# Kernel optimization log

Hardware: AMD Instinct MI355X
Metric: run time of the kernel (lower is better)

Reference implementation:

```python
import jax, jax.numpy as jnp
import numpy as np

NUM_HEADS = 12
SIZE_PER_HEAD = 64


def setup_inputs() -> dict:
    key = jax.random.key(0)
    ks = jax.random.split(key, 4)
    B, S, D = 4, 2048, NUM_HEADS * SIZE_PER_HEAD
    std = 0.02
    return {
        "x": jax.random.normal(ks[0], (B, S, D), dtype=jnp.float32),
        "Wq": jax.random.normal(ks[1], (D, D), dtype=jnp.float32) * std,
        "bq": jnp.zeros((D,), dtype=jnp.float32),
        "Wk": jax.random.normal(ks[2], (D, D), dtype=jnp.float32) * std,
        "bk": jnp.zeros((D,), dtype=jnp.float32),
        "Wv": jax.random.normal(ks[3], (D, D), dtype=jnp.float32) * std,
        "bv": jnp.zeros((D,), dtype=jnp.float32),
        "mask": jnp.ones((B, S), dtype=jnp.int32),
    }


def reference(x, Wq, bq, Wk, bk, Wv, bv, mask):
    B, S, Dm = x.shape
    H, Dh = NUM_HEADS, SIZE_PER_HEAD
    # QKV projections (no activation, per defaults)
    q = (x @ Wq + bq).reshape(B, S, H, Dh)
    k = (x @ Wk + bk).reshape(B, S, H, Dh)
    v = (x @ Wv + bv).reshape(B, S, H, Dh)
    # scaled dot-product scores [B, H, F, T]
    scores = jnp.einsum("bfhd,bthd->bhft", q, k) / jnp.sqrt(
        jnp.asarray(Dh, dtype=x.dtype)
    )
    # additive mask: (1 - mask) * -10000, broadcast over heads and F
    adder = (1.0 - mask.astype(x.dtype))[:, None, None, :] * -10000.0
    probs = jax.nn.softmax(scores + adder, axis=-1)
    # dropout is identity at inference (training=None)
    ctx = jnp.einsum("bhft,bthd->bfhd", probs, v)
    return ctx.reshape(B, S, H * Dh)
```

## Files before the change

kernel.cpp:

```cpp
#include <hip/hip_runtime.h>
#include <cstdint>
#include <cstddef>

#define B_  4
#define S_  2048
#define H_  12
#define DH  64
#define DM  768

typedef unsigned short u16;
typedef __bf16 bf16x8 __attribute__((ext_vector_type(8)));
typedef float f32x4 __attribute__((ext_vector_type(4)));

__device__ __forceinline__ u16 f2bf(float f) {
  unsigned u = __float_as_uint(f);
  u += 0x7FFFu + ((u >> 16) & 1u);
  return (u16)(u >> 16);
}

__device__ __forceinline__ void gl16(const u16* g, u16* l) {
  __builtin_amdgcn_global_load_lds((const __attribute__((address_space(1))) void*)g,
                                   (__attribute__((address_space(3))) void*)l,
                                   16, 0, 0);
}

__global__ __launch_bounds__(256) void k_cvt_x(const float* __restrict__ x, u16* __restrict__ xb,
                                               const int* __restrict__ mask, int* __restrict__ mflags) {
  int i = blockIdx.x * 256 + threadIdx.x;
  const float4 v = ((const float4*)x)[i];
  ushort4 o;
  o.x = f2bf(v.x); o.y = f2bf(v.y); o.z = f2bf(v.z); o.w = f2bf(v.w);
  ((ushort4*)xb)[i] = o;
  if (blockIdx.x < 64) {
    __shared__ int f;
    if (threadIdx.x == 0) f = 0;
    __syncthreads();
    if (threadIdx.x < 128 && mask[blockIdx.x * 128 + threadIdx.x] != 1) f = 1;
    __syncthreads();
    if (threadIdx.x == 0) mflags[blockIdx.x] = f;
  }
}

__global__ __launch_bounds__(256) void k_wtrans(const float* __restrict__ Wq, const float* __restrict__ Wk,
                                                const float* __restrict__ Wv, u16* __restrict__ Wt) {
  const float* W = blockIdx.z == 0 ? Wq : (blockIdx.z == 1 ? Wk : Wv);
  u16* o = Wt + (size_t)blockIdx.z * DM * DM;
  __shared__ float t[32][33];
  const int x = threadIdx.x, y = threadIdx.y;
  const int n0 = blockIdx.x * 32, k0 = blockIdx.y * 32;
#pragma unroll
  for (int i = 0; i < 4; i++)
    t[y + i*8][x] = W[(size_t)(k0 + y + i*8)*DM + n0 + x];
  __syncthreads();
#pragma unroll
  for (int i = 0; i < 4; i++)
    o[(size_t)(n0 + y + i*8)*DM + k0 + x] = f2bf(t[x][y + i*8]);
}

__global__ __launch_bounds__(256) void k_qkv(const u16* __restrict__ Xb, const u16* __restrict__ Wt,
                                             const float* __restrict__ bq, const float* __restrict__ bk,
                                             const float* __restrict__ bv, u16* __restrict__ QKV,
                                             u16* __restrict__ Vt) {
  const int mat = blockIdx.z;
  const float* bias = mat == 0 ? bq : (mat == 1 ? bk : bv);
  const int n0 = blockIdx.x * 128, m0 = blockIdx.y * 128;
  __shared__ __align__(16) u16 Al[128*64];
  __shared__ __align__(16) u16 Bl[128*64];
  const int tid = threadIdx.x, w = tid >> 6, l = tid & 63, l15 = l & 15, quad = l >> 4;
  const int wm = w & 1, wn = w >> 1;
  f32x4 acc[4][4];
#pragma unroll
  for (int i = 0; i < 4; i++)
#pragma unroll
    for (int j = 0; j < 4; j++) acc[i][j] = f32x4{0.f, 0.f, 0.f, 0.f};

  int loff[4];
#pragma unroll
  for (int i = 0; i < 4; i++) {
    int c = tid + i*256;
    int r = c >> 3, s = c & 7, sl = s ^ (r & 7);
    loff[i] = r*DM + sl*8;
  }
  const u16* ap = Xb + (size_t)m0 * DM;
  const u16* bp = Wt + (size_t)mat * DM * DM + (size_t)n0 * DM;

  for (int kt = 0; kt < DM/64; ++kt) {
    __syncthreads();
#pragma unroll
    for (int i = 0; i < 4; i++) {
      int c = tid + i*256;
      gl16(ap + loff[i], Al + c*8);
      gl16(bp + loff[i], Bl + c*8);
    }
    ap += 64; bp += 64;
    __syncthreads();
#pragma unroll
    for (int ks = 0; ks < 2; ++ks) {
      bf16x8 af[4], bfr[4];
#pragma unroll
      for (int mt = 0; mt < 4; mt++) {
        int row = wm*64 + mt*16 + l15;
        int ph = (ks*4 + quad) ^ (row & 7);
        af[mt] = *(const bf16x8*)(Al + row*64 + ph*8);
      }
#pragma unroll
      for (int nt = 0; nt < 4; nt++) {
        int row = wn*64 + nt*16 + l15;
        int ph = (ks*4 + quad) ^ (row & 7);
        bfr[nt] = *(const bf16x8*)(Bl + row*64 + ph*8);
      }
#pragma unroll
      for (int mt = 0; mt < 4; mt++)
#pragma unroll
        for (int nt = 0; nt < 4; nt++)
          acc[mt][nt] = __builtin_amdgcn_mfma_f32_16x16x32_bf16(af[mt], bfr[nt], acc[mt][nt], 0, 0, 0);
    }
  }

  float b4[4];
#pragma unroll
  for (int nt = 0; nt < 4; nt++) b4[nt] = bias[n0 + wn*64 + nt*16 + l15];

  if (mat == 2) {
    const int b = m0 / S_;
    const int h = (n0 + wn*64) >> 6;
    const int tbase = (m0 % S_) + wm*64;
#pragma unroll
    for (int mt = 0; mt < 4; mt++)
#pragma unroll
      for (int nt = 0; nt < 4; nt++) {
        int d = nt*16 + l15;
        int t = tbase + mt*16 + quad*4;
        ushort4 o;
        o.x = f2bf(acc[mt][nt][0] + b4[nt]);
        o.y = f2bf(acc[mt][nt][1] + b4[nt]);
        o.z = f2bf(acc[mt][nt][2] + b4[nt]);
        o.w = f2bf(acc[mt][nt][3] + b4[nt]);
        *(ushort4*)(Vt + ((size_t)(b*H_ + h)*DH + d)*S_ + t) = o;
      }
  } else {
    const float osc = (mat == 0) ? (0.125f * 1.44269504f) : 1.0f;
    u16* outm = QKV + (size_t)mat * (size_t)(B_*S_) * DM;
#pragma unroll
    for (int mt = 0; mt < 4; mt++)
#pragma unroll
      for (int r = 0; r < 4; r++) {
        int gm = m0 + wm*64 + mt*16 + quad*4 + r;
        u16* orow = outm + (size_t)gm*DM + n0 + wn*64;
#pragma unroll
        for (int nt = 0; nt < 4; nt++)
          orow[nt*16 + l15] = f2bf((acc[mt][nt][r] + b4[nt]) * osc);
      }
  }
}

__global__ __launch_bounds__(256, 3) void k_attn(const u16* __restrict__ Qb, const u16* __restrict__ Kb,
                                                 const u16* __restrict__ Vt, const int* __restrict__ mask,
                                                 const int* __restrict__ mflags, float* __restrict__ out) {
  const int bh = blockIdx.x, b = bh / H_, h = bh % H_;
  const int q0 = blockIdx.y * 128;
  __shared__ __align__(16) u16 Kl[128*64];
  __shared__ __align__(16) u16 Vl[64*128];
  __shared__ __align__(16) u16 QP[4*32*72];
  __shared__ __align__(16) float maskl[128];
  const int tid = threadIdx.x, w = tid >> 6, l = tid & 63, l15 = l & 15, quad = l >> 4;

#pragma unroll
  for (int i = 0; i < 4; i++) {
    int c = tid + i*256;
    int r = c >> 3, s = c & 7, sl = s ^ (r & 7);
    gl16(Qb + (size_t)(b*S_ + q0 + r)*DM + h*DH + sl*8, QP + c*8);
  }
  __syncthreads();
  bf16x8 qf[2][2];
#pragma unroll
  for (int nt = 0; nt < 2; nt++)
#pragma unroll
    for (int ks = 0; ks < 2; ks++) {
      int r = w*32 + nt*16 + l15;
      int ph = (ks*4 + quad) ^ (r & 7);
      qf[nt][ks] = *(const bf16x8*)(QP + r*64 + ph*8);
    }
  __syncthreads();

  f32x4 O[2][4], Ol[2];
#pragma unroll
  for (int i = 0; i < 2; i++) {
    Ol[i] = f32x4{0.f, 0.f, 0.f, 0.f};
#pragma unroll
    for (int j = 0; j < 4; j++) O[i][j] = f32x4{0.f, 0.f, 0.f, 0.f};
  }
  const f32x4 ZV = {0.f, 0.f, 0.f, 0.f};
  bf16x8 vone;
#pragma unroll
  for (int j = 0; j < 8; j++) vone[j] = (l15 == 0) ? (__bf16)1.0f : (__bf16)0.0f;
  u16* Pw = QP + w*32*72;

  int koff[4], voff[4];
#pragma unroll
  for (int i = 0; i < 4; i++) {
    int c = tid + i*256;
    { int r = c >> 3, s = c & 7, sl = s ^ (r & 7);   koff[i] = r*DM + sl*8; }
    { int r = c >> 4, s = c & 15, sl = s ^ (r & 15); voff[i] = r*S_ + sl*8; }
  }
  const u16* kp = Kb + (size_t)(b*S_)*DM + h*DH;
  const u16* vp = Vt + (size_t)bh*DH*S_;

  for (int tt = 0; tt < S_/128; ++tt) {
    __syncthreads();
#pragma unroll
    for (int i = 0; i < 4; i++) {
      int c = tid + i*256;
      gl16(kp + koff[i], Kl + c*8);
      gl16(vp + voff[i], Vl + c*8);
    }
    kp += 128*DM; vp += 128;
    const int mflag = mflags[b*16 + tt];
    if (mflag) {
      if (tid < 128)
        maskl[tid] = (1.0f - (float)mask[b*S_ + tt*128 + tid]) * (-10000.0f * 1.44269504f);
    }
    __syncthreads();

#pragma unroll
    for (int h2 = 0; h2 < 2; ++h2) {
      f32x4 sc[4][2];
#pragma unroll
      for (int mt = 0; mt < 4; mt++) {
        int row = h2*64 + mt*16 + l15;
        bf16x8 k0f = *(const bf16x8*)(Kl + row*64 + ((quad    ) ^ (row & 7))*8);
        bf16x8 k1f = *(const bf16x8*)(Kl + row*64 + ((4 + quad) ^ (row & 7))*8);
#pragma unroll
        for (int nt = 0; nt < 2; nt++) {
          sc[mt][nt] = __builtin_amdgcn_mfma_f32_16x16x32_bf16(k0f, qf[nt][0], ZV, 0, 0, 0);
          sc[mt][nt] = __builtin_amdgcn_mfma_f32_16x16x32_bf16(k1f, qf[nt][1], sc[mt][nt], 0, 0, 0);
        }
      }
      if (mflag) {
#pragma unroll
        for (int mt = 0; mt < 4; mt++) {
          f32x4 mv = *(const f32x4*)&maskl[h2*64 + mt*16 + quad*4];
#pragma unroll
          for (int nt = 0; nt < 2; nt++)
#pragma unroll
            for (int r = 0; r < 4; r++) sc[mt][nt][r] += mv[r];
        }
      }
#pragma unroll
      for (int nt = 0; nt < 2; nt++)
#pragma unroll
        for (int mt = 0; mt < 4; mt++) {
          unsigned u[4];
#pragma unroll
          for (int r = 0; r < 4; r++) u[r] = __float_as_uint(exp2f(sc[mt][nt][r]));
          uint2 pk;
          pk.x = __builtin_amdgcn_perm(u[1], u[0], 0x07060302u);
          pk.y = __builtin_amdgcn_perm(u[3], u[2], 0x07060302u);
          *(uint2*)(Pw + (nt*16 + l15)*72 + mt*16 + quad*4) = pk;
        }
      asm volatile("s_waitcnt lgkmcnt(0)" ::: "memory");
#pragma unroll
      for (int kk = 0; kk < 2; kk++) {
        int ksg = h2*2 + kk;
        bf16x8 pa[2], vb[4];
#pragma unroll
        for (int mo = 0; mo < 2; mo++)
          pa[mo] = *(const bf16x8*)(Pw + (mo*16 + l15)*72 + kk*32 + quad*8);
#pragma unroll
        for (int nd = 0; nd < 4; nd++) {
          int d = nd*16 + l15;
          int ph = (ksg*4 + quad) ^ (d & 15);
          vb[nd] = *(const bf16x8*)(Vl + d*128 + ph*8);
        }
#pragma unroll
        for (int mo = 0; mo < 2; mo++) {
#pragma unroll
          for (int nd = 0; nd < 4; nd++)
            O[mo][nd] = __builtin_amdgcn_mfma_f32_16x16x32_bf16(pa[mo], vb[nd], O[mo][nd], 0, 0, 0);
          Ol[mo] = __builtin_amdgcn_mfma_f32_16x16x32_bf16(pa[mo], vone, Ol[mo], 0, 0, 0);
        }
      }
    }
  }

#pragma unroll
  for (int mo = 0; mo < 2; mo++)
#pragma unroll
    for (int r = 0; r < 4; r++) {
      float lsum = __shfl(Ol[mo][r], l & 48);
      float inv = 1.0f / lsum;
      int q = q0 + w*32 + mo*16 + quad*4 + r;
      float* orow = out + (size_t)(b*S_ + q)*DM + h*DH;
#pragma unroll
      for (int nd = 0; nd < 4; nd++)
        orow[nd*16 + l15] = O[mo][nd][r] * inv;
    }
}

extern "C" void kernel_launch(void* const* d_in, const int* in_sizes, int n_in,
                              void* d_out, int out_size, void* d_ws, size_t ws_size,
                              hipStream_t stream) {
  const float* x  = (const float*)d_in[0];
  const float* Wq = (const float*)d_in[1];
  const float* bq = (const float*)d_in[2];
  const float* Wk = (const float*)d_in[3];
  const float* bk = (const float*)d_in[4];
  const float* Wv = (const float*)d_in[5];
  const float* bv = (const float*)d_in[6];
  const int* mask = (const int*)d_in[7];
  float* out = (float*)d_out;

  u16* Xb  = (u16*)d_ws;
  u16* Wt  = Xb  + (size_t)B_*S_*DM;
  u16* QKV = Wt  + (size_t)3*DM*DM;
  u16* Vt  = QKV + (size_t)3*B_*S_*DM;
  int* mflags = (int*)(Vt + (size_t)B_*S_*DM);

  k_cvt_x <<<dim3((B_*S_*DM)/1024), dim3(256), 0, stream>>>(x, Xb, mask, mflags);
  k_wtrans<<<dim3(24, 24, 3), dim3(32, 8), 0, stream>>>(Wq, Wk, Wv, Wt);
  k_qkv   <<<dim3(6, 64, 3), dim3(256), 0, stream>>>(Xb, Wt, bq, bk, bv, QKV, Vt);
  k_attn  <<<dim3(B_*H_, S_/128), dim3(256), 0, stream>>>(QKV, QKV + (size_t)B_*S_*DM, Vt, mask, mflags, out);
}
```

Before: 216.5 us.

## Double-buffer QKV GEMM tiles and widen attention waves to 64 query rows

The QKV projection GEMM now uses a two-stage LDS ring with K-tiles of 32 and a new swizzle, so global loads for the next tile overlap the MFMAs on the current one. It also sets a 4-block occupancy hint. The attention kernel drops to 128 threads with two waves, each handling 64 query rows, which doubles reuse of every K/V fragment read from LDS. It also switches to the raw hardware exp2. The trade-off is more accumulator registers per wave, fewer waves per block to hide latency, and a heavier load loop per thread.

After: 210.7 us. -2.7%, faster.

```diff
diff --git a/kernel.cpp b/kernel.cpp
--- a/kernel.cpp
+++ b/kernel.cpp
@@ -57,15 +57,15 @@
     o[(size_t)(n0 + y + i*8)*DM + k0 + x] = f2bf(t[x][y + i*8]);
 }
 
-__global__ __launch_bounds__(256) void k_qkv(const u16* __restrict__ Xb, const u16* __restrict__ Wt,
-                                             const float* __restrict__ bq, const float* __restrict__ bk,
-                                             const float* __restrict__ bv, u16* __restrict__ QKV,
-                                             u16* __restrict__ Vt) {
+__global__ __launch_bounds__(256, 4) void k_qkv(const u16* __restrict__ Xb, const u16* __restrict__ Wt,
+                                                const float* __restrict__ bq, const float* __restrict__ bk,
+                                                const float* __restrict__ bv, u16* __restrict__ QKV,
+                                                u16* __restrict__ Vt) {
   const int mat = blockIdx.z;
   const float* bias = mat == 0 ? bq : (mat == 1 ? bk : bv);
   const int n0 = blockIdx.x * 128, m0 = blockIdx.y * 128;
-  __shared__ __align__(16) u16 Al[128*64];
-  __shared__ __align__(16) u16 Bl[128*64];
+  __shared__ __align__(16) u16 Al[2*128*32];
+  __shared__ __align__(16) u16 Bl[2*128*32];
   const int tid = threadIdx.x, w = tid >> 6, l = tid & 63, l15 = l & 15, quad = l >> 4;
   const int wm = w & 1, wn = w >> 1;
   f32x4 acc[4][4];
@@ -74,48 +74,51 @@
 #pragma unroll
     for (int j = 0; j < 4; j++) acc[i][j] = f32x4{0.f, 0.f, 0.f, 0.f};
 
-  int loff[4];
-#pragma unroll
-  for (int i = 0; i < 4; i++) {
+  int loff[2], ldst[2];
+#pragma unroll
+  for (int i = 0; i < 2; i++) {
     int c = tid + i*256;
-    int r = c >> 3, s = c & 7, sl = s ^ (r & 7);
+    int r = c >> 2, s = c & 3, sl = s ^ ((r ^ (r >> 2)) & 3);
     loff[i] = r*DM + sl*8;
+    ldst[i] = c*8;
   }
   const u16* ap = Xb + (size_t)m0 * DM;
   const u16* bp = Wt + (size_t)mat * DM * DM + (size_t)n0 * DM;
 
-  for (int kt = 0; kt < DM/64; ++kt) {
-    __syncthreads();
-#pragma unroll
-    for (int i = 0; i < 4; i++) {
-      int c = tid + i*256;
-      gl16(ap + loff[i], Al + c*8);
-      gl16(bp + loff[i], Bl + c*8);
-    }
-    ap += 64; bp += 64;
-    __syncthreads();
-#pragma unroll
-    for (int ks = 0; ks < 2; ++ks) {
-      bf16x8 af[4], bfr[4];
-#pragma unroll
-      for (int mt = 0; mt < 4; mt++) {
-        int row = wm*64 + mt*16 + l15;
-        int ph = (ks*4 + quad) ^ (row & 7);
-        af[mt] = *(const bf16x8*)(Al + row*64 + ph*8);
-      }
-#pragma unroll
-      for (int nt = 0; nt < 4; nt++) {
-        int row = wn*64 + nt*16 + l15;
-        int ph = (ks*4 + quad) ^ (row & 7);
-        bfr[nt] = *(const bf16x8*)(Bl + row*64 + ph*8);
-      }
-#pragma unroll
-      for (int mt = 0; mt < 4; mt++)
-#pragma unroll
-        for (int nt = 0; nt < 4; nt++)
-          acc[mt][nt] = __builtin_amdgcn_mfma_f32_16x16x32_bf16(af[mt], bfr[nt], acc[mt][nt], 0, 0, 0);
-    }
-  }
+#define STAGE(kt) {                                     \
+    int bb = ((kt) & 1) * 4096;                         \
+    _Pragma("unroll")                                   \
+    for (int i = 0; i < 2; i++) {                       \
+      gl16(ap + (kt)*32 + loff[i], Al + bb + ldst[i]);  \
+      gl16(bp + (kt)*32 + loff[i], Bl + bb + ldst[i]);  \
+    }                                                   \
+  }
+
+  STAGE(0)
+  for (int kt = 0; kt < DM/32; ++kt) {
+    __syncthreads();
+    if (kt + 1 < DM/32) STAGE(kt+1)
+    const int bb = (kt & 1) * 4096;
+    bf16x8 af[4], bfr[4];
+#pragma unroll
+    for (int mt = 0; mt < 4; mt++) {
+      int row = wm*64 + mt*16 + l15;
+      int ph = quad ^ ((row ^ (row >> 2)) & 3);
+      af[mt] = *(const bf16x8*)(Al + bb + row*32 + ph*8);
+    }
+#pragma unroll
+    for (int nt = 0; nt < 4; nt++) {
+      int row = wn*64 + nt*16 + l15;
+      int ph = quad ^ ((row ^ (row >> 2)) & 3);
+      bfr[nt] = *(const bf16x8*)(Bl + bb + row*32 + ph*8);
+    }
+#pragma unroll
+    for (int mt = 0; mt < 4; mt++)
+#pragma unroll
+      for (int nt = 0; nt < 4; nt++)
+        acc[mt][nt] = __builtin_amdgcn_mfma_f32_16x16x32_bf16(af[mt], bfr[nt], acc[mt][nt], 0, 0, 0);
+  }
+#undef STAGE
 
   float b4[4];
 #pragma unroll
@@ -154,38 +157,38 @@
   }
 }
 
-__global__ __launch_bounds__(256, 3) void k_attn(const u16* __restrict__ Qb, const u16* __restrict__ Kb,
+__global__ __launch_bounds__(128, 2) void k_attn(const u16* __restrict__ Qb, const u16* __restrict__ Kb,
                                                  const u16* __restrict__ Vt, const int* __restrict__ mask,
                                                  const int* __restrict__ mflags, float* __restrict__ out) {
   const int bh = blockIdx.x, b = bh / H_, h = bh % H_;
   const int q0 = blockIdx.y * 128;
   __shared__ __align__(16) u16 Kl[128*64];
   __shared__ __align__(16) u16 Vl[64*128];
-  __shared__ __align__(16) u16 QP[4*32*72];
+  __shared__ __align__(16) u16 QP[2*64*72];
   __shared__ __align__(16) float maskl[128];
   const int tid = threadIdx.x, w = tid >> 6, l = tid & 63, l15 = l & 15, quad = l >> 4;
 
 #pragma unroll
-  for (int i = 0; i < 4; i++) {
-    int c = tid + i*256;
+  for (int i = 0; i < 8; i++) {
+    int c = tid + i*128;
     int r = c >> 3, s = c & 7, sl = s ^ (r & 7);
     gl16(Qb + (size_t)(b*S_ + q0 + r)*DM + h*DH + sl*8, QP + c*8);
   }
   __syncthreads();
-  bf16x8 qf[2][2];
-#pragma unroll
-  for (int nt = 0; nt < 2; nt++)
+  bf16x8 qf[4][2];
+#pragma unroll
+  for (int nt = 0; nt < 4; nt++)
 #pragma unroll
     for (int ks = 0; ks < 2; ks++) {
-      int r = w*32 + nt*16 + l15;
+      int r = w*64 + nt*16 + l15;
       int ph = (ks*4 + quad) ^ (r & 7);
       qf[nt][ks] = *(const bf16x8*)(QP + r*64 + ph*8);
     }
   __syncthreads();
 
-  f32x4 O[2][4], Ol[2];
-#pragma unroll
-  for (int i = 0; i < 2; i++) {
+  f32x4 O[4][4], Ol[4];
+#pragma unroll
+  for (int i = 0; i < 4; i++) {
     Ol[i] = f32x4{0.f, 0.f, 0.f, 0.f};
 #pragma unroll
     for (int j = 0; j < 4; j++) O[i][j] = f32x4{0.f, 0.f, 0.f, 0.f};
@@ -194,12 +197,12 @@
   bf16x8 vone;
 #pragma unroll
   for (int j = 0; j < 8; j++) vone[j] = (l15 == 0) ? (__bf16)1.0f : (__bf16)0.0f;
-  u16* Pw = QP + w*32*72;
-
-  int koff[4], voff[4];
-#pragma unroll
-  for (int i = 0; i < 4; i++) {
-    int c = tid + i*256;
+  u16* Pw = QP + w*64*72;
+
+  int koff[8], voff[8];
+#pragma unroll
+  for (int i = 0; i < 8; i++) {
+    int c = tid + i*128;
     { int r = c >> 3, s = c & 7, sl = s ^ (r & 7);   koff[i] = r*DM + sl*8; }
     { int r = c >> 4, s = c & 15, sl = s ^ (r & 15); voff[i] = r*S_ + sl*8; }
   }
@@ -209,29 +212,27 @@
   for (int tt = 0; tt < S_/128; ++tt) {
     __syncthreads();
 #pragma unroll
-    for (int i = 0; i < 4; i++) {
-      int c = tid + i*256;
+    for (int i = 0; i < 8; i++) {
+      int c = tid + i*128;
       gl16(kp + koff[i], Kl + c*8);
       gl16(vp + voff[i], Vl + c*8);
     }
     kp += 128*DM; vp += 128;
     const int mflag = mflags[b*16 + tt];
-    if (mflag) {
-      if (tid < 128)
-        maskl[tid] = (1.0f - (float)mask[b*S_ + tt*128 + tid]) * (-10000.0f * 1.44269504f);
-    }
+    if (mflag)
+      maskl[tid] = (1.0f - (float)mask[b*S_ + tt*128 + tid]) * (-10000.0f * 1.44269504f);
     __syncthreads();
 
 #pragma unroll
     for (int h2 = 0; h2 < 2; ++h2) {
-      f32x4 sc[4][2];
+      f32x4 sc[4][4];
 #pragma unroll
       for (int mt = 0; mt < 4; mt++) {
         int row = h2*64 + mt*16 + l15;
         bf16x8 k0f = *(const bf16x8*)(Kl + row*64 + ((quad    ) ^ (row & 7))*8);
         bf16x8 k1f = *(const bf16x8*)(Kl + row*64 + ((4 + quad) ^ (row & 7))*8);
 #pragma unroll
-        for (int nt = 0; nt < 2; nt++) {
+        for (int nt = 0; nt < 4; nt++) {
           sc[mt][nt] = __builtin_amdgcn_mfma_f32_16x16x32_bf16(k0f, qf[nt][0], ZV, 0, 0, 0);
           sc[mt][nt] = __builtin_amdgcn_mfma_f32_16x16x32_bf16(k1f, qf[nt][1], sc[mt][nt], 0, 0, 0);
         }
@@ -241,18 +242,18 @@
         for (int mt = 0; mt < 4; mt++) {
           f32x4 mv = *(const f32x4*)&maskl[h2*64 + mt*16 + quad*4];
 #pragma unroll
-          for (int nt = 0; nt < 2; nt++)
+          for (int nt = 0; nt < 4; nt++)
 #pragma unroll
             for (int r = 0; r < 4; r++) sc[mt][nt][r] += mv[r];
         }
       }
 #pragma unroll
-      for (int nt = 0; nt < 2; nt++)
+      for (int nt = 0; nt < 4; nt++)
 #pragma unroll
         for (int mt = 0; mt < 4; mt++) {
           unsigned u[4];
 #pragma unroll
-          for (int r = 0; r < 4; r++) u[r] = __float_as_uint(exp2f(sc[mt][nt][r]));
+          for (int r = 0; r < 4; r++) u[r] = __float_as_uint(__builtin_amdgcn_exp2f(sc[mt][nt][r]));
           uint2 pk;
           pk.x = __builtin_amdgcn_perm(u[1], u[0], 0x07060302u);
           pk.y = __builtin_amdgcn_perm(u[3], u[2], 0x07060302u);
@@ -262,9 +263,9 @@
 #pragma unroll
       for (int kk = 0; kk < 2; kk++) {
         int ksg = h2*2 + kk;
-        bf16x8 pa[2], vb[4];
-#pragma unroll
-        for (int mo = 0; mo < 2; mo++)
+        bf16x8 pa[4], vb[4];
+#pragma unroll
+        for (int mo = 0; mo < 4; mo++)
           pa[mo] = *(const bf16x8*)(Pw + (mo*16 + l15)*72 + kk*32 + quad*8);
 #pragma unroll
         for (int nd = 0; nd < 4; nd++) {
@@ -273,7 +274,7 @@
           vb[nd] = *(const bf16x8*)(Vl + d*128 + ph*8);
         }
 #pragma unroll
-        for (int mo = 0; mo < 2; mo++) {
+        for (int mo = 0; mo < 4; mo++) {
 #pragma unroll
           for (int nd = 0; nd < 4; nd++)
             O[mo][nd] = __builtin_amdgcn_mfma_f32_16x16x32_bf16(pa[mo], vb[nd], O[mo][nd], 0, 0, 0);
@@ -284,12 +285,12 @@
   }
 
 #pragma unroll
-  for (int mo = 0; mo < 2; mo++)
+  for (int mo = 0; mo < 4; mo++)
 #pragma unroll
     for (int r = 0; r < 4; r++) {
       float lsum = __shfl(Ol[mo][r], l & 48);
       float inv = 1.0f / lsum;
-      int q = q0 + w*32 + mo*16 + quad*4 + r;
+      int q = q0 + w*64 + mo*16 + quad*4 + r;
       float* orow = out + (size_t)(b*S_ + q)*DM + h*DH;
 #pragma unroll
       for (int nd = 0; nd < 4; nd++)
@@ -319,5 +320,5 @@
   k_cvt_x <<<dim3((B_*S_*DM)/1024), dim3(256), 0, stream>>>(x, Xb, mask, mflags);
   k_wtrans<<<dim3(24, 24, 3), dim3(32, 8), 0, stream>>>(Wq, Wk, Wv, Wt);
   k_qkv   <<<dim3(6, 64, 3), dim3(256), 0, stream>>>(Xb, Wt, bq, bk, bv, QKV, Vt);
-  k_attn  <<<dim3(B_*H_, S_/128), dim3(256), 0, stream>>>(QKV, QKV + (size_t)B_*S_*DM, Vt, mask, mflags, out);
-}
+  k_attn  <<<dim3(B_*H_, S_/128), dim3(128), 0, stream>>>(QKV, QKV + (size_t)B_*S_*DM, Vt, mask, mflags, out);
+}
```
